# Optimization experiments

Hardware: AMD Instinct MI355X
Metric: run time of the kernel (lower is better)

Reference implementation:

```python
import jax, jax.numpy as jnp
import numpy as np

NEG = -1.0e9  # matches the -1000000000.0 masking constant in the torch source


def setup_inputs() -> dict:
    key = jax.random.key(0)
    k1, k2, k3, k4 = jax.random.split(key, 4)
    B, N, M, D = 32, 2048, 512, 128
    sequence1 = jax.random.normal(k1, (B, N, D), dtype=jnp.float32)
    sequence2 = jax.random.normal(k2, (B, M, D), dtype=jnp.float32)
    sequence1_mask = jax.random.randint(k3, (B, N), 0, 2, dtype=jnp.int32)
    sequence2_mask = jax.random.randint(k4, (B, M), 0, 2, dtype=jnp.int32)
    return {
        "sequence1": sequence1,
        "sequence2": sequence2,
        "sequence1_mask": sequence1_mask,
        "sequence2_mask": sequence2_mask,
    }


def reference(sequence1, sequence2, sequence1_mask, sequence2_mask):
    # sequence1: [B, n, d] (context), sequence2: [B, m, d] (question)
    dt = sequence1.dtype
    m1 = sequence1_mask.astype(dt)  # [B, n]
    m2 = sequence2_mask.astype(dt)  # [B, m]

    # DotProduct similarity over the (virtually) tiled tensors -> [B, n, m].
    # Fused: no [B,n,m,d] intermediates.
    S = jnp.einsum('bnd,bmd->bnm', sequence1, sequence2)

    # masked softmax over sequence2 positions (context-to-question attention)
    a2 = jax.nn.softmax(S + (1.0 - m2)[:, None, :] * NEG, axis=-1)  # [B, n, m]
    seq1_seq2_attention = jnp.einsum('bnm,bmd->bnd', a2, sequence2)

    # one-shot question-to-context attention: masked max over m, softmax over n
    s1 = jnp.max(S * m2[:, None, :] + (1.0 - m2)[:, None, :] * NEG, axis=-1)  # [B, n]
    a1 = jax.nn.softmax(s1 + (1.0 - m1) * NEG, axis=-1)  # [B, n]
    seq2_seq1_attention = jnp.einsum('bn,bnd->bd', a1, sequence1)  # [B, d]

    return (seq1_seq2_attention, a2, seq2_seq1_attention, a1)
```

## Files before the change

kernel.cpp:

```cpp
#include <hip/hip_runtime.h>
#include <stdint.h>

#define NEGC (-1.0e9f)

typedef __attribute__((ext_vector_type(8))) short bf16x8;
typedef __attribute__((ext_vector_type(4))) float f32x4;

__device__ __align__(16) unsigned short g_S2H[32u * 512u * 128u];
__device__ __align__(16) unsigned short g_S2L[32u * 512u * 128u];
__device__ __align__(16) unsigned short g_VF[32u * 128u * 512u];

__device__ __forceinline__ unsigned short f2bf(float f) {
    union { float f; unsigned int u; } v; v.f = f;
    unsigned int r = v.u + 0x7fffu + ((v.u >> 16) & 1u);
    return (unsigned short)(r >> 16);
}
__device__ __forceinline__ float bf2f(unsigned short h) {
    union { float f; unsigned int u; } v; v.u = ((unsigned int)h) << 16;
    return v.f;
}

__device__ __forceinline__ void gl_lds16(const void* g, void* l) {
    __builtin_amdgcn_global_load_lds(
        (const __attribute__((address_space(1))) unsigned int*)g,
        (__attribute__((address_space(3))) unsigned int*)l, 16, 0, 0);
}

__global__ __launch_bounds__(256) void k_prep(const float* __restrict__ seq2) {
    __shared__ unsigned short Lh[32 * 136];
    const int b = blockIdx.x >> 4, c = blockIdx.x & 15, t = threadIdx.x;
    const int m0 = c * 32;

    const float4* src = (const float4*)(seq2 + (size_t)(b * 512 + m0) * 128);
    ushort4* dh = (ushort4*)(g_S2H + (size_t)(b * 512 + m0) * 128);
    ushort4* dl = (ushort4*)(g_S2L + (size_t)(b * 512 + m0) * 128);
#pragma unroll
    for (int p = 0; p < 4; ++p) {
        int idx = p * 256 + t;
        int row = idx >> 5, c4 = idx & 31;
        float4 v = src[idx];
        float vs[4] = {v.x, v.y, v.z, v.w};
        unsigned short hh[4], ll[4];
#pragma unroll
        for (int i = 0; i < 4; ++i) { hh[i] = f2bf(vs[i]); ll[i] = f2bf(vs[i] - bf2f(hh[i])); }
        ushort4 uh{hh[0], hh[1], hh[2], hh[3]};
        ushort4 ul{ll[0], ll[1], ll[2], ll[3]};
        dh[idx] = uh;
        dl[idx] = ul;
#pragma unroll
        for (int i = 0; i < 4; ++i) Lh[row * 136 + c4 * 4 + i] = hh[i];
    }
    __syncthreads();

    {
        const int l = t & 63, q = (t >> 4) & 3, fr = t & 15;
        const int ms = m0 >> 5;
#pragma unroll
        for (int pass = 0; pass < 2; ++pass) {
            int id = pass * 4 + (t >> 6);
            int wcd = id >> 2, cc = id & 3;
            int d = wcd * 64 + cc * 16 + fr;
            unsigned short pk[8];
#pragma unroll
            for (int j = 0; j < 8; ++j) pk[j] = Lh[(q * 8 + j) * 136 + d];
            size_t chunk = (size_t)b * 65536 + (size_t)wcd * 32768
                         + (size_t)ms * 2048 + cc * 512 + l * 8;
            *(bf16x8*)(g_VF + chunk) = *(bf16x8*)pk;
        }
    }
}

#define LDS_TOTAL 32768

__global__ __launch_bounds__(256, 4) void bidir_main(
    const float* __restrict__ seq1,
    const int* __restrict__ m1, const int* __restrict__ m2,
    float* __restrict__ out0, float* __restrict__ a2out,
    float* __restrict__ a1log)
{
    __shared__ __align__(16) char smem[LDS_TOTAL];

    const int t = threadIdx.x, lane = t & 63, w = t >> 6;
    const int wr = w >> 1, wc = w & 1, q = lane >> 4, fr = lane & 15;
    const int orig = blockIdx.x;
    const int swzb = (orig & 7) * 256 + (orig >> 3);
    const int b = swzb >> 6, n0 = (swzb & 63) << 5;

    float* REDm = (float*)(smem);
    float* REDs = (float*)(smem + 256);

    auto stageK = [&](int buf, int kt) {
        const unsigned short* sb = (w < 2) ? g_S2H : g_S2L;
        const int h = w & 1;
        const char* srcb = (const char*)(sb + (size_t)(b * 512 + h * 256 + kt * 16) * 128);
        char* dstb = smem + buf * 16384 + (w >> 1) * 8192 + h * 4096;
#pragma unroll
        for (int i = 0; i < 4; ++i) {
            int r = i * 4 + q;
            int so = r * 256 + ((fr * 16) ^ ((r & 7) << 4));
            gl_lds16(srcb + so, dstb + i * 1024);
        }
    };

    stageK(0, 0);

    bf16x8 ah[4], al[4];
    {
        const float* qp = seq1 + (size_t)(b * 2048 + n0 + wr * 16 + fr) * 128;
#pragma unroll
        for (int ks = 0; ks < 4; ++ks) {
            float4 v0 = *(const float4*)(qp + ks * 32 + q * 8);
            float4 v1 = *(const float4*)(qp + ks * 32 + q * 8 + 4);
            float vs[8] = {v0.x, v0.y, v0.z, v0.w, v1.x, v1.y, v1.z, v1.w};
            unsigned short hh[8], ll[8];
#pragma unroll
            for (int j = 0; j < 8; ++j) { hh[j] = f2bf(vs[j]); ll[j] = f2bf(vs[j] - bf2f(hh[j])); }
            ah[ks] = *(bf16x8*)hh;
            al[ks] = *(bf16x8*)ll;
        }
    }

    f32x4 acc[8][2];
#pragma unroll
    for (int i = 0; i < 8; ++i) {
        acc[i][0] = (f32x4){0.f, 0.f, 0.f, 0.f};
        acc[i][1] = (f32x4){0.f, 0.f, 0.f, 0.f};
    }

    __syncthreads();

#pragma unroll
    for (int kt = 0; kt < 16; ++kt) {
        if (kt < 15) stageK((kt + 1) & 1, kt + 1);
        {
            const char* KH = smem + (kt & 1) * 16384;
            const char* KL = KH + 8192;
            const int rrow = wc * 16 + fr;
            const int sw = (fr & 7) << 4;
            f32x4 a = acc[kt >> 1][kt & 1];
#pragma unroll
            for (int ks = 0; ks < 4; ++ks) {
                int off = (rrow * 256 + ks * 64 + q * 16) ^ sw;
                bf16x8 bh = *(const bf16x8*)(KH + off);
                bf16x8 bl = *(const bf16x8*)(KL + off);
                a = __builtin_amdgcn_mfma_f32_16x16x32_bf16(al[ks], bh, a, 0, 0, 0);
                a = __builtin_amdgcn_mfma_f32_16x16x32_bf16(ah[ks], bl, a, 0, 0, 0);
                a = __builtin_amdgcn_mfma_f32_16x16x32_bf16(ah[ks], bh, a, 0, 0, 0);
            }
            acc[kt >> 1][kt & 1] = a;
        }
        __syncthreads();
    }

    {
        const int* m2p = m2 + b * 512 + wc * 256 + fr;
#pragma unroll
        for (int mt = 0; mt < 8; ++mt)
#pragma unroll
            for (int s = 0; s < 2; ++s) {
                bool keep = m2p[mt * 32 + s * 16] != 0;
#pragma unroll
                for (int r = 0; r < 4; ++r)
                    acc[mt][s][r] = keep ? acc[mt][s][r] : NEGC;
            }
    }
    float rmax[4];
#pragma unroll
    for (int r = 0; r < 4; ++r) rmax[r] = NEGC;
#pragma unroll
    for (int mt = 0; mt < 8; ++mt)
#pragma unroll
        for (int s = 0; s < 2; ++s)
#pragma unroll
            for (int r = 0; r < 4; ++r) rmax[r] = fmaxf(rmax[r], acc[mt][s][r]);
#pragma unroll
    for (int off = 1; off < 16; off <<= 1)
#pragma unroll
        for (int r = 0; r < 4; ++r) rmax[r] = fmaxf(rmax[r], __shfl_xor(rmax[r], off));
    if (fr == 0) {
#pragma unroll
        for (int r = 0; r < 4; ++r) REDm[wc * 32 + wr * 16 + q * 4 + r] = rmax[r];
    }
    __syncthreads();
    float RM[4];
#pragma unroll
    for (int r = 0; r < 4; ++r) {
        int rl = wr * 16 + q * 4 + r;
        RM[r] = fmaxf(REDm[rl], REDm[32 + rl]);
    }
    if (t < 32) {
        float v = fmaxf(REDm[t], REDm[32 + t]);
        float m1v = (float)m1[b * 2048 + n0 + t];
        a1log[b * 2048 + n0 + t] = v + (1.0f - m1v) * NEGC;
    }
    float rs[4] = {0.f, 0.f, 0.f, 0.f};
#pragma unroll
    for (int mt = 0; mt < 8; ++mt)
#pragma unroll
        for (int s = 0; s < 2; ++s)
#pragma unroll
            for (int r = 0; r < 4; ++r) {
                float e = __expf(acc[mt][s][r] - RM[r]);
                acc[mt][s][r] = e;
                rs[r] += e;
            }
#pragma unroll
    for (int off = 1; off < 16; off <<= 1)
#pragma unroll
        for (int r = 0; r < 4; ++r) rs[r] += __shfl_xor(rs[r], off);
    if (fr == 0) {
#pragma unroll
        for (int r = 0; r < 4; ++r) REDs[wc * 32 + wr * 16 + q * 4 + r] = rs[r];
    }
    __syncthreads();
    float rinv[4];
#pragma unroll
    for (int r = 0; r < 4; ++r) {
        int rl = wr * 16 + q * 4 + r;
        rinv[r] = 1.0f / (REDs[rl] + REDs[32 + rl]);
    }
    __syncthreads();

#pragma unroll
    for (int mt = 0; mt < 8; ++mt)
#pragma unroll
        for (int s = 0; s < 2; ++s) {
            int m = wc * 256 + mt * 32 + s * 16 + fr;
#pragma unroll
            for (int r = 0; r < 4; ++r) {
                int rl = wr * 16 + q * 4 + r;
                float v = acc[mt][s][r] * rinv[r];
                a2out[(size_t)(b * 2048 + n0 + rl) * 512 + m] = v;
                int off = (rl * 1024 + m * 2) ^ ((rl & 7) << 4);
                *(unsigned short*)(smem + off) = f2bf(v);
            }
        }
    __syncthreads();

    f32x4 oacc[4];
#pragma unroll
    for (int c = 0; c < 4; ++c) oacc[c] = (f32x4){0.f, 0.f, 0.f, 0.f};

    {
        const unsigned short* vf = g_VF + (size_t)b * 65536 + (size_t)wc * 32768 + lane * 8;
        const int arow = wr * 16 + fr;
        const int asw = (fr & 7) << 4;
#pragma unroll
        for (int ms = 0; ms < 16; ++ms) {
            bf16x8 bv[4];
#pragma unroll
            for (int c = 0; c < 4; ++c)
                bv[c] = *(const bf16x8*)(vf + ms * 2048 + c * 512);
            int aoff = (arow * 1024 + ms * 64 + q * 16) ^ asw;
            bf16x8 pa = *(const bf16x8*)(smem + aoff);
#pragma unroll
            for (int c = 0; c < 4; ++c)
                oacc[c] = __builtin_amdgcn_mfma_f32_16x16x32_bf16(pa, bv[c], oacc[c], 0, 0, 0);
        }
    }

#pragma unroll
    for (int c = 0; c < 4; ++c)
#pragma unroll
        for (int r = 0; r < 4; ++r) {
            int rl = wr * 16 + q * 4 + r;
            int d = wc * 64 + c * 16 + fr;
            out0[(size_t)(b * 2048 + n0 + rl) * 128 + d] = oacc[c][r];
        }
}

__global__ __launch_bounds__(256) void k_a1(float* __restrict__ a1slot,
                                            float* __restrict__ out2) {
    __shared__ float wred[4];
    const int b = blockIdx.x, t = threadIdx.x, lane = t & 63, w = t >> 6;

    if (t < 128) out2[b * 128 + t] = 0.f;

    const float4* Lp = (const float4*)(a1slot + (size_t)b * 2048);
    float4 La = Lp[t * 2], Lb = Lp[t * 2 + 1];
    float l[8] = {La.x, La.y, La.z, La.w, Lb.x, Lb.y, Lb.z, Lb.w};

    float lmax = l[0];
#pragma unroll
    for (int j = 1; j < 8; ++j) lmax = fmaxf(lmax, l[j]);
#pragma unroll
    for (int off = 1; off < 64; off <<= 1) lmax = fmaxf(lmax, __shfl_xor(lmax, off));
    if (lane == 0) wred[w] = lmax;
    __syncthreads();
    float bmax = fmaxf(fmaxf(wred[0], wred[1]), fmaxf(wred[2], wred[3]));

    float e[8]; float s = 0.f;
#pragma unroll
    for (int j = 0; j < 8; ++j) { e[j] = __expf(l[j] - bmax); s += e[j]; }
#pragma unroll
    for (int off = 1; off < 64; off <<= 1) s += __shfl_xor(s, off);
    __syncthreads();
    if (lane == 0) wred[w] = s;
    __syncthreads();
    float inv = 1.0f / (wred[0] + wred[1] + wred[2] + wred[3]);

    float4 o1{e[0] * inv, e[1] * inv, e[2] * inv, e[3] * inv};
    float4 o2v{e[4] * inv, e[5] * inv, e[6] * inv, e[7] * inv};
    ((float4*)(a1slot + (size_t)b * 2048))[t * 2] = o1;
    ((float4*)(a1slot + (size_t)b * 2048))[t * 2 + 1] = o2v;
}

__global__ __launch_bounds__(256) void k_gemv(const float* __restrict__ seq1,
                                              const float* __restrict__ a1,
                                              float* __restrict__ out2) {
    __shared__ float a1b[256];
    __shared__ float4 red[8][32];
    const int bid = blockIdx.x, b = bid >> 3, ch = bid & 7, t = threadIdx.x;
    const int n0 = ch * 256;
    if (t < 64) ((float4*)a1b)[t] = ((const float4*)(a1 + (size_t)b * 2048 + n0))[t];
    __syncthreads();
    const int d4 = t & 31, sl = t >> 5;
    float4 acc{0.f, 0.f, 0.f, 0.f};
    const float4* s1 = (const float4*)(seq1 + (size_t)(b * 2048 + n0 + sl * 32) * 128);
#pragma unroll 8
    for (int j = 0; j < 32; ++j) {
        float wv = a1b[sl * 32 + j];
        float4 v = s1[j * 32 + d4];
        acc.x += wv * v.x; acc.y += wv * v.y; acc.z += wv * v.z; acc.w += wv * v.w;
    }
    red[sl][d4] = acc;
    __syncthreads();
    if (t < 32) {
        float4 s0 = red[0][t];
#pragma unroll
        for (int c = 1; c < 8; ++c) {
            float4 v = red[c][t];
            s0.x += v.x; s0.y += v.y; s0.z += v.z; s0.w += v.w;
        }
        float* dst = out2 + b * 128 + t * 4;
        atomicAdd(dst + 0, s0.x);
        atomicAdd(dst + 1, s0.y);
        atomicAdd(dst + 2, s0.z);
        atomicAdd(dst + 3, s0.w);
    }
}

extern "C" void kernel_launch(void* const* d_in, const int* in_sizes, int n_in,
                              void* d_out, int out_size, void* d_ws, size_t ws_size,
                              hipStream_t stream) {
    const float* seq1 = (const float*)d_in[0];
    const float* seq2 = (const float*)d_in[1];
    const int*   m1   = (const int*)d_in[2];
    const int*   m2   = (const int*)d_in[3];
    (void)d_ws; (void)ws_size; (void)n_in; (void)in_sizes;

    float* out  = (float*)d_out;
    float* out0 = out;
    float* a2o  = out + 8388608;
    float* o2   = out + 41943040;
    float* a1o  = out + 41947136;

    k_prep<<<dim3(512), dim3(256), 0, stream>>>(seq2);
    bidir_main<<<dim3(2048), dim3(256), 0, stream>>>(seq1, m1, m2, out0, a2o, a1o);
    k_a1<<<dim3(32), dim3(256), 0, stream>>>(a1o, o2);
    k_gemv<<<dim3(256), dim3(256), 0, stream>>>(seq1, a1o, o2);
}
```

Measured before the change: 82.38 us.

## Coalesce a2 stores via LDS readback and fold a1 softmax into gemv

The a2 probabilities are no longer written to global memory as scattered 4-byte stores straight from the MFMA accumulator layout. Each row is read back from the swizzled bf16 LDS tile and written as contiguous float4 stores, so the largest output gets wide, coalesced writes. The separate k_a1 kernel is removed: each k_gemv block recomputes the batch softmax over a1 logits held in a device global, and the out2 zeroing moves into the main kernel, saving one launch. The risk is precision: a2 is now emitted at bf16 precision instead of fp32, and the a1 softmax is computed redundantly in every gemv block.

```diff
diff --git a/kernel.cpp b/kernel.cpp
--- a/kernel.cpp
+++ b/kernel.cpp
@@ -9,6 +9,7 @@
 __device__ __align__(16) unsigned short g_S2H[32u * 512u * 128u];
 __device__ __align__(16) unsigned short g_S2L[32u * 512u * 128u];
 __device__ __align__(16) unsigned short g_VF[32u * 128u * 512u];
+__device__ float g_a1log[32 * 2048];
 
 __device__ __forceinline__ unsigned short f2bf(float f) {
     union { float f; unsigned int u; } v; v.f = f;
@@ -76,7 +77,7 @@
     const float* __restrict__ seq1,
     const int* __restrict__ m1, const int* __restrict__ m2,
     float* __restrict__ out0, float* __restrict__ a2out,
-    float* __restrict__ a1log)
+    float* __restrict__ out2)
 {
     __shared__ __align__(16) char smem[LDS_TOTAL];
 
@@ -88,6 +89,11 @@
 
     float* REDm = (float*)(smem);
     float* REDs = (float*)(smem + 256);
+
+    if (orig == 0) {
+#pragma unroll
+        for (int i = 0; i < 16; ++i) out2[i * 256 + t] = 0.f;
+    }
 
     auto stageK = [&](int buf, int kt) {
         const unsigned short* sb = (w < 2) ? g_S2H : g_S2L;
@@ -191,7 +197,7 @@
     if (t < 32) {
         float v = fmaxf(REDm[t], REDm[32 + t]);
         float m1v = (float)m1[b * 2048 + n0 + t];
-        a1log[b * 2048 + n0 + t] = v + (1.0f - m1v) * NEGC;
+        g_a1log[b * 2048 + n0 + t] = v + (1.0f - m1v) * NEGC;
     }
     float rs[4] = {0.f, 0.f, 0.f, 0.f};
 #pragma unroll
@@ -229,13 +235,30 @@
 #pragma unroll
             for (int r = 0; r < 4; ++r) {
                 int rl = wr * 16 + q * 4 + r;
-                float v = acc[mt][s][r] * rinv[r];
-                a2out[(size_t)(b * 2048 + n0 + rl) * 512 + m] = v;
                 int off = (rl * 1024 + m * 2) ^ ((rl & 7) << 4);
-                *(unsigned short*)(smem + off) = f2bf(v);
+                *(unsigned short*)(smem + off) = f2bf(acc[mt][s][r] * rinv[r]);
             }
         }
     __syncthreads();
+
+#pragma unroll
+    for (int i = 0; i < 8; ++i) {
+        int rl = w * 8 + i;
+        int off = (rl * 1024 + lane * 16) ^ ((rl & 7) << 4);
+        bf16x8 hv = *(const bf16x8*)(smem + off);
+        float fv[8];
+#pragma unroll
+        for (int j = 0; j < 8; ++j) {
+            union { float f; unsigned int u; } cv;
+            cv.u = ((unsigned int)(unsigned short)hv[j]) << 16;
+            fv[j] = cv.f;
+        }
+        float4 o0{fv[0], fv[1], fv[2], fv[3]};
+        float4 o1{fv[4], fv[5], fv[6], fv[7]};
+        float4* dst = (float4*)(a2out + (size_t)(b * 2048 + n0 + rl) * 512 + lane * 8);
+        dst[0] = o0;
+        dst[1] = o1;
+    }
 
     f32x4 oacc[4];
 #pragma unroll
@@ -269,51 +292,51 @@
         }
 }
 
-__global__ __launch_bounds__(256) void k_a1(float* __restrict__ a1slot,
-                                            float* __restrict__ out2) {
-    __shared__ float wred[4];
-    const int b = blockIdx.x, t = threadIdx.x, lane = t & 63, w = t >> 6;
-
-    if (t < 128) out2[b * 128 + t] = 0.f;
-
-    const float4* Lp = (const float4*)(a1slot + (size_t)b * 2048);
-    float4 La = Lp[t * 2], Lb = Lp[t * 2 + 1];
-    float l[8] = {La.x, La.y, La.z, La.w, Lb.x, Lb.y, Lb.z, Lb.w};
-
-    float lmax = l[0];
-#pragma unroll
-    for (int j = 1; j < 8; ++j) lmax = fmaxf(lmax, l[j]);
-#pragma unroll
-    for (int off = 1; off < 64; off <<= 1) lmax = fmaxf(lmax, __shfl_xor(lmax, off));
-    if (lane == 0) wred[w] = lmax;
-    __syncthreads();
-    float bmax = fmaxf(fmaxf(wred[0], wred[1]), fmaxf(wred[2], wred[3]));
-
-    float e[8]; float s = 0.f;
-#pragma unroll
-    for (int j = 0; j < 8; ++j) { e[j] = __expf(l[j] - bmax); s += e[j]; }
-#pragma unroll
-    for (int off = 1; off < 64; off <<= 1) s += __shfl_xor(s, off);
-    __syncthreads();
-    if (lane == 0) wred[w] = s;
-    __syncthreads();
-    float inv = 1.0f / (wred[0] + wred[1] + wred[2] + wred[3]);
-
-    float4 o1{e[0] * inv, e[1] * inv, e[2] * inv, e[3] * inv};
-    float4 o2v{e[4] * inv, e[5] * inv, e[6] * inv, e[7] * inv};
-    ((float4*)(a1slot + (size_t)b * 2048))[t * 2] = o1;
-    ((float4*)(a1slot + (size_t)b * 2048))[t * 2 + 1] = o2v;
-}
-
 __global__ __launch_bounds__(256) void k_gemv(const float* __restrict__ seq1,
-                                              const float* __restrict__ a1,
+                                              float* __restrict__ a1out,
                                               float* __restrict__ out2) {
     __shared__ float a1b[256];
     __shared__ float4 red[8][32];
+    __shared__ float wred[4];
     const int bid = blockIdx.x, b = bid >> 3, ch = bid & 7, t = threadIdx.x;
+    const int lane = t & 63, w = t >> 6;
     const int n0 = ch * 256;
-    if (t < 64) ((float4*)a1b)[t] = ((const float4*)(a1 + (size_t)b * 2048 + n0))[t];
-    __syncthreads();
+
+    const float4* Lp = (const float4*)(g_a1log + (size_t)b * 2048);
+    float4 La = Lp[t * 2], Lb = Lp[t * 2 + 1];
+    float l[8] = {La.x, La.y, La.z, La.w, Lb.x, Lb.y, Lb.z, Lb.w};
+
+    float lmax = l[0];
+#pragma unroll
+    for (int j = 1; j < 8; ++j) lmax = fmaxf(lmax, l[j]);
+#pragma unroll
+    for (int off = 1; off < 64; off <<= 1) lmax = fmaxf(lmax, __shfl_xor(lmax, off));
+    if (lane == 0) wred[w] = lmax;
+    __syncthreads();
+    float bmax = fmaxf(fmaxf(wred[0], wred[1]), fmaxf(wred[2], wred[3]));
+
+    float e[8]; float s = 0.f;
+#pragma unroll
+    for (int j = 0; j < 8; ++j) { e[j] = __expf(l[j] - bmax); s += e[j]; }
+#pragma unroll
+    for (int off = 1; off < 64; off <<= 1) s += __shfl_xor(s, off);
+    __syncthreads();
+    if (lane == 0) wred[w] = s;
+    __syncthreads();
+    float inv = 1.0f / (wred[0] + wred[1] + wred[2] + wred[3]);
+
+    if ((t >> 5) == ch) {
+        float4 w0{e[0] * inv, e[1] * inv, e[2] * inv, e[3] * inv};
+        float4 w1{e[4] * inv, e[5] * inv, e[6] * inv, e[7] * inv};
+        int li = (t - ch * 32) * 8;
+        *(float4*)(a1b + li) = w0;
+        *(float4*)(a1b + li + 4) = w1;
+        float4* ao = (float4*)(a1out + (size_t)b * 2048 + t * 8);
+        ao[0] = w0;
+        ao[1] = w1;
+    }
+    __syncthreads();
+
     const int d4 = t & 31, sl = t >> 5;
     float4 acc{0.f, 0.f, 0.f, 0.f};
     const float4* s1 = (const float4*)(seq1 + (size_t)(b * 2048 + n0 + sl * 32) * 128);
@@ -356,7 +379,6 @@
     float* a1o  = out + 41947136;
 
     k_prep<<<dim3(512), dim3(256), 0, stream>>>(seq2);
-    bidir_main<<<dim3(2048), dim3(256), 0, stream>>>(seq1, m1, m2, out0, a2o, a1o);
-    k_a1<<<dim3(32), dim3(256), 0, stream>>>(a1o, o2);
+    bidir_main<<<dim3(2048), dim3(256), 0, stream>>>(seq1, m1, m2, out0, a2o, o2);
     k_gemv<<<dim3(256), dim3(256), 0, stream>>>(seq1, a1o, o2);
 }
```

Result: slower. 88.18 us (+7.0%).
